# Kernel tuning notes

Measured on AMD Instinct MI355X. Metric: run time of the kernel, lower is better.

The kernel has to match this reference:

```python
import jax, jax.numpy as jnp
import numpy as np

N_NODES = 50000
N_EDGES = 600000
H = 128


def setup_inputs() -> dict:
    key = jax.random.key(0)
    ks = jax.random.split(key, 7)
    node_emb = jax.random.normal(ks[0], (N_NODES, H), dtype=jnp.float32)
    # PyTorch Linear default init ~ U(-1/sqrt(fan_in), 1/sqrt(fan_in)); scaled normal is fine for a baseline
    W1 = jax.random.normal(ks[1], (H, 2 * H), dtype=jnp.float32) * (1.0 / np.sqrt(2 * H))
    b1 = jax.random.normal(ks[2], (H,), dtype=jnp.float32) * 0.01
    W2 = jax.random.normal(ks[3], (1, H), dtype=jnp.float32) * (1.0 / np.sqrt(H))
    b2 = jax.random.normal(ks[4], (1,), dtype=jnp.float32) * 0.01
    src = jax.random.randint(ks[5], (N_EDGES,), 0, N_NODES, dtype=jnp.int64)
    dst = jax.random.randint(ks[6], (N_EDGES,), 0, N_NODES, dtype=jnp.int64)
    return {"node_emb": node_emb, "W1": W1, "b1": b1, "W2": W2, "b2": b2,
            "src": src, "dst": dst}


def reference(node_emb, W1, b1, W2, b2, src, dst):
    # gather per-edge endpoint embeddings and concat -> [E, 2H]
    h = jnp.concatenate([node_emb[src], node_emb[dst]], axis=1)
    # 2-layer MLP: Linear(2H->H) -> ReLU -> Linear(H->1) -> squeeze
    hidden = jax.nn.relu(h @ W1.T + b1)          # [E, H]
    scores = hidden @ W2.T + b2                   # [E, 1]
    return scores[:, 0]                           # [E]
```

## Files before the change

### kernel.cpp

```cpp
#include <hip/hip_runtime.h>
#include <hip/hip_bf16.h>


#define H   128
#define NJJ 256
#define BM  32
#define EPW 32
#define CPAD_F32 264

typedef __attribute__((ext_vector_type(8))) short  frag_ab;
typedef __attribute__((ext_vector_type(4))) float  f32x4;
typedef __attribute__((ext_vector_type(8))) unsigned short ushort8;
typedef __attribute__((ext_vector_type(4))) unsigned int   uint4v;

__device__ __forceinline__ unsigned short f2bf(float x) {
    unsigned int u = __float_as_uint(x);
    unsigned int r = u + 0x7FFFu + ((u >> 16) & 1u);
    return (unsigned short)(r >> 16);
}

__device__ __forceinline__ unsigned int pk_bf16(float lo, float hi) {
    unsigned int r;
    asm("v_cvt_pk_bf16_f32 %0, %1, %2" : "=v"(r) : "v"(lo), "v"(hi));
    return r;
}

__device__ __forceinline__ frag_ab relu_sum(uint4v s, uint4v d) {
    uint4v r;
#pragma unroll
    for (int p = 0; p < 4; ++p) {
        float sl = __uint_as_float(s[p] << 16);
        float sh = __uint_as_float(s[p] & 0xFFFF0000u);
        float dl = __uint_as_float(d[p] << 16);
        float dh = __uint_as_float(d[p] & 0xFFFF0000u);
        float l = sl + dl; l = l > 0.f ? l : 0.f;
        float h = sh + dh; h = h > 0.f ? h : 0.f;
        r[p] = pk_bf16(l, h);
    }
    return __builtin_bit_cast(frag_ab, r);
}

__global__ __launch_bounds__(256)
void convert_weights(const float* __restrict__ W1, const float* __restrict__ W2,
                     unsigned short* __restrict__ W1f, unsigned short* __restrict__ W2c) {
    if (blockIdx.x == 128) {
        if (threadIdx.x < H) W2c[threadIdx.x] = f2bf(W2[threadIdx.x]);
        return;
    }
    int idx = blockIdx.x * 256 + threadIdx.x;
    int e     = idx & 7;
    int chunk = idx >> 3;
    int lane  = chunk & 63;
    int ks    = (chunk >> 6) & 3;
    int cf    = (chunk >> 8) & 3;
    int wid   = chunk >> 10;
    int col   = wid * 64 + (lane & 15) + cf * 16;
    int k     = ks * 32 + (lane >> 4) * 8 + e;
    W1f[idx] = f2bf(W1[(size_t)(col & 127) * 256 + (size_t)(col >> 7) * H + k]);
}

__global__ __launch_bounds__(256, 4)
void precompute_P_mfma(const float* __restrict__ emb,
                       const unsigned short* __restrict__ W1f,
                       const float* __restrict__ b1,
                       unsigned short* __restrict__ P,
                       int n_nodes) {
    __shared__ __align__(16) char ldsbuf[BM * CPAD_F32 * 4];
    unsigned short* ldsA = (unsigned short*)ldsbuf;
    float* ldsC = (float*)ldsbuf;

    int tid  = threadIdx.x;
    int lane = tid & 63;
    int wid  = tid >> 6;
    int block0 = blockIdx.x * BM;
    if (block0 + BM > n_nodes) block0 = n_nodes - BM;
    if (block0 < 0) block0 = 0;

    {
        int row = tid >> 3;
        int q   = tid & 7;
        int grow = block0 + row;
        const float4* src = (const float4*)(emb + (size_t)grow * H + q * 16);
#pragma unroll
        for (int i = 0; i < 2; ++i) {
            float4 a = src[2 * i], b = src[2 * i + 1];
            ushort8 v;
            v[0] = f2bf(a.x); v[1] = f2bf(a.y); v[2] = f2bf(a.z); v[3] = f2bf(a.w);
            v[4] = f2bf(b.x); v[5] = f2bf(b.y); v[6] = f2bf(b.z); v[7] = f2bf(b.w);
            int k0 = q * 16 + i * 8;
            int byte = (row * 256 + k0 * 2) ^ ((row & 7) << 4);
            *(ushort8*)((char*)ldsA + byte) = v;
        }
    }
    __syncthreads();

    const frag_ab* wf = (const frag_ab*)W1f;
    f32x4 acc[2][4];
#pragma unroll
    for (int mf = 0; mf < 2; ++mf)
#pragma unroll
        for (int cf = 0; cf < 4; ++cf) acc[mf][cf] = (f32x4){0.f, 0.f, 0.f, 0.f};

    frag_ab Bcur[4], Bnxt[4];
#pragma unroll
    for (int cf = 0; cf < 4; ++cf)
        Bcur[cf] = wf[((wid * 4 + cf) * 4 + 0) * 64 + lane];

#pragma unroll
    for (int ks = 0; ks < 4; ++ks) {
        if (ks < 3) {
#pragma unroll
            for (int cf = 0; cf < 4; ++cf)
                Bnxt[cf] = wf[((wid * 4 + cf) * 4 + ks + 1) * 64 + lane];
        }
        frag_ab Af[2];
#pragma unroll
        for (int mf = 0; mf < 2; ++mf) {
            int row = mf * 16 + (lane & 15);
            int k   = ks * 32 + (lane >> 4) * 8;
            int byte = (row * 256 + k * 2) ^ ((row & 7) << 4);
            Af[mf] = *(const frag_ab*)((const char*)ldsA + byte);
        }
#pragma unroll
        for (int mf = 0; mf < 2; ++mf)
#pragma unroll
            for (int cf = 0; cf < 4; ++cf)
                acc[mf][cf] = __builtin_amdgcn_mfma_f32_16x16x32_bf16(
                    Af[mf], Bcur[cf], acc[mf][cf], 0, 0, 0);
        if (ks < 3) {
#pragma unroll
            for (int cf = 0; cf < 4; ++cf) Bcur[cf] = Bnxt[cf];
        }
    }

    __syncthreads();

    {
        int colbase = wid * 64 + (lane & 15);
        int rbase   = (lane >> 4) * 4;
        float b1c[4];
#pragma unroll
        for (int cf = 0; cf < 4; ++cf) {
            int col = colbase + cf * 16;
            b1c[cf] = (col < H) ? b1[col] : 0.f;
        }
#pragma unroll
        for (int mf = 0; mf < 2; ++mf)
#pragma unroll
            for (int cf = 0; cf < 4; ++cf) {
                int col = colbase + cf * 16;
#pragma unroll
                for (int r = 0; r < 4; ++r) {
                    int row = mf * 16 + rbase + r;
                    ldsC[row * CPAD_F32 + col] = acc[mf][cf][r] + b1c[cf];
                }
            }
    }
    __syncthreads();

#pragma unroll
    for (int it = 0; it < 4; ++it) {
        int c   = it * 256 + tid;
        int row = c >> 5;
        int off = c & 31;
        const float4* s = (const float4*)(ldsC + row * CPAD_F32 + off * 8);
        float4 x = s[0], y = s[1];
        uint4v o;
        o[0] = pk_bf16(x.x, x.y);
        o[1] = pk_bf16(x.z, x.w);
        o[2] = pk_bf16(y.x, y.y);
        o[3] = pk_bf16(y.z, y.w);
        *(uint4v*)((char*)P + (size_t)(block0 + row) * 512 + off * 16) = o;
    }
}

__global__ __launch_bounds__(256)
void edge_score_mfma(const unsigned short* __restrict__ P,
                     const unsigned short* __restrict__ W2c,
                     const float* __restrict__ b2,
                     const int* __restrict__ src,
                     const int* __restrict__ dst,
                     float* __restrict__ out,
                     int n_edges) {
    int lane = threadIdx.x & 63;
    int wave = blockIdx.x * 4 + (threadIdx.x >> 6);
    int e0 = wave * EPW;
    if (e0 >= n_edges) return;

    frag_ab Bf[4];
    {
        int krun = (lane >> 4) * 8;
#pragma unroll
        for (int ks = 0; ks < 4; ++ks)
            Bf[ks] = *(const frag_ab*)(W2c + ks * 32 + krun);
    }
    float b2v = b2[0];
    int el = lane & 15;
    int kb = (lane >> 4) * 16;

    int eA = e0 + el;       if (eA > n_edges - 1) eA = n_edges - 1;
    int eB = e0 + 16 + el;  if (eB > n_edges - 1) eB = n_edges - 1;
    const char* pb = (const char*)P;
    const char* sA = pb + (size_t)src[eA] * 512 + kb;
    const char* dA = pb + (size_t)dst[eA] * 512 + 256 + kb;
    const char* sB = pb + (size_t)src[eB] * 512 + kb;
    const char* dB = pb + (size_t)dst[eB] * 512 + 256 + kb;

    uint4v rsA[4], rdA[4], rsB[4], rdB[4];
#pragma unroll
    for (int ks = 0; ks < 4; ++ks) {
        rsA[ks] = *(const uint4v*)(sA + ks * 64);
        rdA[ks] = *(const uint4v*)(dA + ks * 64);
        rsB[ks] = *(const uint4v*)(sB + ks * 64);
        rdB[ks] = *(const uint4v*)(dB + ks * 64);
    }

    f32x4 accA = (f32x4){0.f, 0.f, 0.f, 0.f};
    f32x4 accB = (f32x4){0.f, 0.f, 0.f, 0.f};
#pragma unroll
    for (int ks = 0; ks < 4; ++ks) {
        accA = __builtin_amdgcn_mfma_f32_16x16x32_bf16(relu_sum(rsA[ks], rdA[ks]), Bf[ks], accA, 0, 0, 0);
        accB = __builtin_amdgcn_mfma_f32_16x16x32_bf16(relu_sum(rsB[ks], rdB[ks]), Bf[ks], accB, 0, 0, 0);
    }

    if (el == 0) {
        int r0 = (lane >> 4) * 4;
        int ea = e0 + r0, eb = e0 + 16 + r0;
        float4 oA = { accA[0] + b2v, accA[1] + b2v, accA[2] + b2v, accA[3] + b2v };
        float4 oB = { accB[0] + b2v, accB[1] + b2v, accB[2] + b2v, accB[3] + b2v };
        if (eb + 3 < n_edges) {
            *(float4*)(out + ea) = oA;
            *(float4*)(out + eb) = oB;
        } else {
#pragma unroll
            for (int r = 0; r < 4; ++r) {
                if (ea + r < n_edges) out[ea + r] = accA[r] + b2v;
                if (eb + r < n_edges) out[eb + r] = accB[r] + b2v;
            }
        }
    }
}

__global__ __launch_bounds__(128)
void naive_edge(const float* __restrict__ emb,
                const float* __restrict__ W1,
                const float* __restrict__ b1,
                const float* __restrict__ W2,
                const float* __restrict__ b2,
                const int* __restrict__ src,
                const int* __restrict__ dst,
                float* __restrict__ out,
                int n_edges) {
    __shared__ float es[H], ed[H];
    __shared__ float red[2];
    int e = blockIdx.x;
    if (e >= n_edges) return;
    int j = threadIdx.x;
    int s = src[e], d = dst[e];
    es[j] = emb[(size_t)s * H + j];
    ed[j] = emb[(size_t)d * H + j];
    __syncthreads();
    const float* w = W1 + (size_t)j * 256;
    float acc = b1[j];
    for (int k = 0; k < H; ++k) acc += es[k] * w[k] + ed[k] * w[H + k];
    acc = acc > 0.f ? acc : 0.f;
    float p = acc * W2[j];
#pragma unroll
    for (int off = 32; off; off >>= 1) p += __shfl_xor(p, off, 64);
    int lane = j & 63, wid = j >> 6;
    if (lane == 0) red[wid] = p;
    __syncthreads();
    if (j == 0) out[e] = red[0] + red[1] + b2[0];
}

extern "C" void kernel_launch(void* const* d_in, const int* in_sizes, int n_in,
                              void* d_out, int out_size, void* d_ws, size_t ws_size,
                              hipStream_t stream) {
    const float* emb = (const float*)d_in[0];
    const float* W1  = (const float*)d_in[1];
    const float* b1  = (const float*)d_in[2];
    const float* W2  = (const float*)d_in[3];
    const float* b2  = (const float*)d_in[4];
    const int*   src = (const int*)d_in[5];
    const int*   dst = (const int*)d_in[6];
    float* out = (float*)d_out;

    int n_nodes = in_sizes[0] / H;
    int n_edges = in_sizes[5];

    size_t needP = (size_t)n_nodes * NJJ * sizeof(unsigned short);
    size_t offW1 = (needP + 255) & ~(size_t)255;
    size_t offW2 = offW1 + (size_t)NJJ * H * sizeof(unsigned short);
    size_t need  = offW2 + 256;

    if (ws_size >= need && n_nodes >= BM) {
        unsigned short* P   = (unsigned short*)d_ws;
        unsigned short* W1f = (unsigned short*)((char*)d_ws + offW1);
        unsigned short* W2c = (unsigned short*)((char*)d_ws + offW2);
        convert_weights<<<129, 256, 0, stream>>>(W1, W2, W1f, W2c);
        int grid1 = (n_nodes + BM - 1) / BM;
        precompute_P_mfma<<<grid1, 256, 0, stream>>>(emb, W1f, b1, P, n_nodes);
        int grid2 = (n_edges + EPW * 4 - 1) / (EPW * 4);
        edge_score_mfma<<<grid2, 256, 0, stream>>>(P, W2c, b2, src, dst, out, n_edges);
    } else {
        naive_edge<<<n_edges, 128, 0, stream>>>(emb, W1, b1, W2, b2, src, dst, out, n_edges);
    }
}
```

Baseline: 66.55 us.

## Load A fragments directly from global memory, skipping LDS staging in precompute

The precompute kernel no longer stages node embeddings through LDS with a swizzled bf16 layout. Each lane now reads its A-fragment straight from global memory and packs it with v_cvt_pk_bf16_f32. All W1 B-fragments are preloaded into registers up front instead of being double-buffered, and the barrier around the old LDS stage is gone. The launch-bounds occupancy hint is dropped and the LDS padding changed, trading extra redundant global reads (each embedding row is loaded by all four waves) and higher register use for fewer syncs and less LDS traffic.

Result: slower. 73.02 us (+9.7%).

```diff
diff --git a/kernel.cpp b/kernel.cpp
--- a/kernel.cpp
+++ b/kernel.cpp
@@ -6,11 +6,10 @@
 #define NJJ 256
 #define BM  32
 #define EPW 32
-#define CPAD_F32 264
+#define CPAD_F32 260
 
 typedef __attribute__((ext_vector_type(8))) short  frag_ab;
 typedef __attribute__((ext_vector_type(4))) float  f32x4;
-typedef __attribute__((ext_vector_type(8))) unsigned short ushort8;
 typedef __attribute__((ext_vector_type(4))) unsigned int   uint4v;
 
 __device__ __forceinline__ unsigned short f2bf(float x) {
@@ -59,16 +58,13 @@
     W1f[idx] = f2bf(W1[(size_t)(col & 127) * 256 + (size_t)(col >> 7) * H + k]);
 }
 
-__global__ __launch_bounds__(256, 4)
+__global__ __launch_bounds__(256)
 void precompute_P_mfma(const float* __restrict__ emb,
                        const unsigned short* __restrict__ W1f,
                        const float* __restrict__ b1,
                        unsigned short* __restrict__ P,
                        int n_nodes) {
-    __shared__ __align__(16) char ldsbuf[BM * CPAD_F32 * 4];
-    unsigned short* ldsA = (unsigned short*)ldsbuf;
-    float* ldsC = (float*)ldsbuf;
-
+    __shared__ __align__(16) float ldsC[BM * CPAD_F32];
     int tid  = threadIdx.x;
     int lane = tid & 63;
     int wid  = tid >> 6;
@@ -76,68 +72,49 @@
     if (block0 + BM > n_nodes) block0 = n_nodes - BM;
     if (block0 < 0) block0 = 0;
 
-    {
-        int row = tid >> 3;
-        int q   = tid & 7;
-        int grow = block0 + row;
-        const float4* src = (const float4*)(emb + (size_t)grow * H + q * 16);
-#pragma unroll
-        for (int i = 0; i < 2; ++i) {
-            float4 a = src[2 * i], b = src[2 * i + 1];
-            ushort8 v;
-            v[0] = f2bf(a.x); v[1] = f2bf(a.y); v[2] = f2bf(a.z); v[3] = f2bf(a.w);
-            v[4] = f2bf(b.x); v[5] = f2bf(b.y); v[6] = f2bf(b.z); v[7] = f2bf(b.w);
-            int k0 = q * 16 + i * 8;
-            int byte = (row * 256 + k0 * 2) ^ ((row & 7) << 4);
-            *(ushort8*)((char*)ldsA + byte) = v;
-        }
-    }
-    __syncthreads();
-
     const frag_ab* wf = (const frag_ab*)W1f;
+    frag_ab Bf[4][4];
+#pragma unroll
+    for (int cf = 0; cf < 4; ++cf)
+#pragma unroll
+        for (int ks = 0; ks < 4; ++ks)
+            Bf[cf][ks] = wf[(((size_t)wid * 4 + cf) * 4 + ks) * 64 + lane];
+
     f32x4 acc[2][4];
 #pragma unroll
     for (int mf = 0; mf < 2; ++mf)
 #pragma unroll
         for (int cf = 0; cf < 4; ++cf) acc[mf][cf] = (f32x4){0.f, 0.f, 0.f, 0.f};
 
-    frag_ab Bcur[4], Bnxt[4];
-#pragma unroll
-    for (int cf = 0; cf < 4; ++cf)
-        Bcur[cf] = wf[((wid * 4 + cf) * 4 + 0) * 64 + lane];
+    int row16 = lane & 15;
+    int g     = lane >> 4;
+    const float* a0 = emb + (size_t)(block0 + row16) * H + g * 8;
 
 #pragma unroll
     for (int ks = 0; ks < 4; ++ks) {
-        if (ks < 3) {
-#pragma unroll
-            for (int cf = 0; cf < 4; ++cf)
-                Bnxt[cf] = wf[((wid * 4 + cf) * 4 + ks + 1) * 64 + lane];
-        }
         frag_ab Af[2];
 #pragma unroll
         for (int mf = 0; mf < 2; ++mf) {
-            int row = mf * 16 + (lane & 15);
-            int k   = ks * 32 + (lane >> 4) * 8;
-            int byte = (row * 256 + k * 2) ^ ((row & 7) << 4);
-            Af[mf] = *(const frag_ab*)((const char*)ldsA + byte);
+            const float4* p = (const float4*)(a0 + mf * 16 * H + ks * 32);
+            float4 a = p[0], b = p[1];
+            uint4v w;
+            w[0] = pk_bf16(a.x, a.y);
+            w[1] = pk_bf16(a.z, a.w);
+            w[2] = pk_bf16(b.x, b.y);
+            w[3] = pk_bf16(b.z, b.w);
+            Af[mf] = __builtin_bit_cast(frag_ab, w);
         }
 #pragma unroll
         for (int mf = 0; mf < 2; ++mf)
 #pragma unroll
             for (int cf = 0; cf < 4; ++cf)
                 acc[mf][cf] = __builtin_amdgcn_mfma_f32_16x16x32_bf16(
-                    Af[mf], Bcur[cf], acc[mf][cf], 0, 0, 0);
-        if (ks < 3) {
-#pragma unroll
-            for (int cf = 0; cf < 4; ++cf) Bcur[cf] = Bnxt[cf];
-        }
-    }
-
-    __syncthreads();
+                    Af[mf], Bf[cf][ks], acc[mf][cf], 0, 0, 0);
+    }
 
     {
-        int colbase = wid * 64 + (lane & 15);
-        int rbase   = (lane >> 4) * 4;
+        int colbase = wid * 64 + row16;
+        int rbase   = g * 4;
         float b1c[4];
 #pragma unroll
         for (int cf = 0; cf < 4; ++cf) {
```
